# Performance work log

Measured on AMD Instinct MI355X. Metric: run time of the kernel, lower is better.

## Reference

```python
import math
import jax, jax.numpy as jnp
import numpy as np

L, C, FC, K, H, WIN, T, B = 6, 512, 2048, 3, 8, 4, 1024, 4
KC = C // H
EPS = 1e-4


def setup_inputs() -> dict:
    key = jax.random.key(0)
    ks = jax.random.split(key, 20)
    s = 0.05
    f = jnp.float32
    inp = {
        "x": jax.random.normal(ks[0], (B, C, T), f),
        "wq": jax.random.normal(ks[1], (L, C, C), f) * s,
        "bq": jnp.zeros((L, C), f),
        "wk": jax.random.normal(ks[2], (L, C, C), f) * s,
        "bk": jnp.zeros((L, C), f),
        "wv": jax.random.normal(ks[3], (L, C, C), f) * s,
        "bv": jnp.zeros((L, C), f),
        "wo": jax.random.normal(ks[4], (L, C, C), f) * s,
        "bo": jnp.zeros((L, C), f),
        "rel_k": jax.random.normal(ks[5], (L, 1, 2 * WIN + 1, KC), f) * (KC ** -0.5),
        "g1": jnp.ones((L, C), f),
        "be1": jnp.zeros((L, C), f),
        "w1": jax.random.normal(ks[6], (L, FC, C, K), f) * s,
        "bb1": jnp.zeros((L, FC), f),
        "w2": jax.random.normal(ks[7], (L, C, FC, K), f) * s,
        "bb2": jnp.zeros((L, C), f),
        "g2": jnp.ones((L, C), f),
        "be2": jnp.zeros((L, C), f),
    }
    return inp


def conv1d(x, w, b, pad):
    # x: [B,Cin,T], w: [Cout,Cin,K]
    y = jax.lax.conv_general_dilated(x, w, (1,), [(pad, pad)],
                                     dimension_numbers=("NCH", "OIH", "NCH"))
    return y + b[None, :, None]


def layer_norm(x, g, b):
    # normalize over channel dim (axis 1), matching the torch LayerNorm above
    m = jnp.mean(x, 1, keepdims=True)
    v = jnp.mean((x - m) ** 2, 1, keepdims=True)
    return (x - m) * jax.lax.rsqrt(v + EPS) * g[None, :, None] + b[None, :, None]


def get_relative_embeddings(rel, length):
    pad_len = max(length - (WIN + 1), 0)
    start = max(WIN + 1 - length, 0)
    if pad_len > 0:
        rel = jnp.pad(rel, ((0, 0), (pad_len, pad_len), (0, 0)), mode="edge")
    return rel[:, start:start + 2 * length - 1]


def rel_to_abs(x):
    # x: [b,h,l,2l-1] -> [b,h,l,l]  (Music-Transformer skew)
    b, h, l, _ = x.shape
    x = jnp.pad(x, ((0, 0), (0, 0), (0, 0), (0, 1)))          # [b,h,l,2l]
    x = x.reshape(b, h, l * 2 * l)
    x = jnp.pad(x, ((0, 0), (0, 0), (0, l - 1)))
    x = x.reshape(b, h, l + 1, 2 * l - 1)[:, :, :l, l - 1:]
    return x


def attention(x, wq, bq, wk, bk, wv, bv, wo, bo, rel_k):
    b, c, t = x.shape
    q = conv1d(x, wq[:, :, None], bq, 0).reshape(b, H, KC, t)
    k = conv1d(x, wk[:, :, None], bk, 0).reshape(b, H, KC, t)
    v = conv1d(x, wv[:, :, None], bv, 0).reshape(b, H, KC, t)
    scale = 1.0 / math.sqrt(KC)
    scores = jnp.einsum("bhdt,bhds->bhts", q, k) * scale      # [b,H,t,t]
    rel = get_relative_embeddings(rel_k, t)[0]                # [2t-1, KC] (heads_share)
    rel_logits = jnp.einsum("bhdt,md->bhtm", q * scale, rel)  # [b,H,t,2t-1]
    scores = scores + rel_to_abs(rel_logits)
    p = jax.nn.softmax(scores, axis=-1)
    out = jnp.einsum("bhts,bhds->bhdt", p, v).reshape(b, c, t)
    return conv1d(out, wo[:, :, None], bo, 0)


def reference(x, wq, bq, wk, bk, wv, bv, wo, bo, rel_k,
              g1, be1, w1, bb1, w2, bb2, g2, be2):
    for i in range(L):
        y = attention(x, wq[i], bq[i], wk[i], bk[i], wv[i], bv[i],
                      wo[i], bo[i], rel_k[i])
        x = layer_norm(x + y, g1[i], be1[i])
        y = conv1d(jax.nn.relu(conv1d(x, w1[i], bb1[i], K // 2)), w2[i], bb2[i], K // 2)
        x = layer_norm(x + y, g2[i], be2[i])
    return x
```

## Files before the change

kernel.cpp:

```cpp
#include <hip/hip_runtime.h>

constexpr int L  = 6;
constexpr int C  = 512;
constexpr int FC = 2048;
constexpr int H  = 8;
constexpr int KC = 64;
constexpr int T  = 1024;
constexpr int B  = 4;
#define SCALE 0.125f
#define LOG2E 1.4426950408889634f

typedef __bf16 bf16_t;
typedef __bf16 bf16x8 __attribute__((ext_vector_type(8)));
typedef float  f32x4  __attribute__((ext_vector_type(4)));

constexpr size_t OFF_XF    = 0;
constexpr size_t OFF_YF    = OFF_XF   + (size_t)B*T*C*4;
constexpr size_t OFF_XPAD  = OFF_YF   + (size_t)B*T*C*4;
constexpr size_t OFF_Q     = OFF_XPAD + (size_t)B*(T+2)*C*2;
constexpr size_t OFF_K     = OFF_Q    + (size_t)B*T*C*2;
constexpr size_t OFF_VT    = OFF_K    + (size_t)B*T*C*2;
constexpr size_t OFF_YA    = OFF_VT   + (size_t)B*T*C*2;
constexpr size_t OFF_MID   = OFF_YA   + (size_t)B*T*C*2;
constexpr size_t OFF_WQKVO = OFF_MID  + (size_t)B*(T+2)*FC*2;
constexpr size_t OFF_W1    = OFF_WQKVO+ (size_t)4*C*C*2;
constexpr size_t OFF_W2    = OFF_W1   + (size_t)3*FC*C*2;

__device__ __forceinline__ void gload_lds16(const bf16_t* g, bf16_t* l) {
    __builtin_amdgcn_global_load_lds((const __attribute__((address_space(1))) void*)g,
                                     (__attribute__((address_space(3))) void*)l, 16, 0, 0);
}

__global__ __launch_bounds__(256) void cvt4_kernel(const float* __restrict__ a,
                                                   const float* __restrict__ b,
                                                   const float* __restrict__ c,
                                                   const float* __restrict__ d,
                                                   bf16_t* __restrict__ out) {
    int i = blockIdx.x * 256 + threadIdx.x;
    int which = i >> 18;
    int idx   = i & ((1 << 18) - 1);
    const float* s = (which == 0) ? a : (which == 1) ? b : (which == 2) ? c : d;
    out[i] = (bf16_t)s[idx];
}

__global__ __launch_bounds__(256) void cvtw1_kernel(const float* __restrict__ w1, bf16_t* __restrict__ out) {
    int i = blockIdx.x * 256 + threadIdx.x;
    int j = i >> 20;
    int rem = i & ((1 << 20) - 1);
    int fc = rem >> 9, c = rem & 511;
    out[i] = (bf16_t)w1[fc * (C * 3) + c * 3 + j];
}

__global__ __launch_bounds__(256) void cvtw2_kernel(const float* __restrict__ w2, bf16_t* __restrict__ out) {
    int i = blockIdx.x * 256 + threadIdx.x;
    int j = i >> 20;
    int rem = i & ((1 << 20) - 1);
    int c = rem >> 11, fc = rem & 2047;
    out[i] = (bf16_t)w2[c * (FC * 3) + fc * 3 + j];
}

__global__ __launch_bounds__(256) void transpose_in(const float* __restrict__ x0,
                                                    float* __restrict__ xf,
                                                    bf16_t* __restrict__ xpad) {
    __shared__ float tile[32][33];
    int b = blockIdx.z, t0 = blockIdx.x * 32, c0 = blockIdx.y * 32;
    int tx = threadIdx.x, ty = threadIdx.y;
#pragma unroll
    for (int j = 0; j < 4; ++j)
        tile[ty + j * 8][tx] = x0[((size_t)b * C + c0 + ty + j * 8) * T + t0 + tx];
    __syncthreads();
#pragma unroll
    for (int j = 0; j < 4; ++j) {
        float v = tile[tx][ty + j * 8];
        long t = t0 + ty + j * 8;
        xf[((size_t)b * T + t) * C + c0 + tx] = v;
        xpad[((size_t)b * (T + 2) + t + 1) * C + c0 + tx] = (bf16_t)v;
    }
}

__global__ __launch_bounds__(256) void transpose_out(const float* __restrict__ xf,
                                                     float* __restrict__ out) {
    __shared__ float tile[32][33];
    int b = blockIdx.z, t0 = blockIdx.x * 32, c0 = blockIdx.y * 32;
    int tx = threadIdx.x, ty = threadIdx.y;
#pragma unroll
    for (int j = 0; j < 4; ++j)
        tile[ty + j * 8][tx] = xf[((size_t)b * T + t0 + ty + j * 8) * C + c0 + tx];
    __syncthreads();
#pragma unroll
    for (int j = 0; j < 4; ++j)
        out[((size_t)b * C + c0 + ty + j * 8) * T + t0 + tx] = tile[tx][ty + j * 8];
}

__global__ __launch_bounds__(256) void zero_pads(bf16_t* __restrict__ xpad, bf16_t* __restrict__ midp) {
    int i = blockIdx.x * 256 + threadIdx.x;
    if (i < 4096) {
        int b = i >> 10, r = (i >> 9) & 1, c = i & 511;
        xpad[((size_t)b * (T + 2) + (size_t)r * (T + 1)) * C + c] = (bf16_t)0.f;
    } else {
        int j = i - 4096;
        int b = j >> 12, r = (j >> 11) & 1, c = j & 2047;
        midp[((size_t)b * (T + 2) + (size_t)r * (T + 1)) * FC + c] = (bf16_t)0.f;
    }
}

template <int NP>
__global__ __launch_bounds__(256) void add_ln(float* __restrict__ x,
                                              const float* __restrict__ p0, const float* __restrict__ p1,
                                              const float* __restrict__ p2,
                                              const float* __restrict__ g, const float* __restrict__ be,
                                              bf16_t* __restrict__ xpad) {
    long bt = blockIdx.x;
    int tid = threadIdx.x;
    float* xr = x + bt * C;
    float v0 = xr[tid] + p0[bt * C + tid] + p1[bt * C + tid];
    float v1 = xr[tid + 256] + p0[bt * C + tid + 256] + p1[bt * C + tid + 256];
    if (NP == 3) { v0 += p2[bt * C + tid]; v1 += p2[bt * C + tid + 256]; }
    float s = v0 + v1, q = v0 * v0 + v1 * v1;
#pragma unroll
    for (int m = 1; m < 64; m <<= 1) { s += __shfl_xor(s, m); q += __shfl_xor(q, m); }
    __shared__ float ss[4], qq[4];
    int wid = tid >> 6;
    if ((tid & 63) == 0) { ss[wid] = s; qq[wid] = q; }
    __syncthreads();
    s = ss[0] + ss[1] + ss[2] + ss[3];
    q = qq[0] + qq[1] + qq[2] + qq[3];
    float mean = s * (1.f / C);
    float var = q * (1.f / C) - mean * mean;
    float rstd = rsqrtf(var + 1e-4f);
    float o0 = (v0 - mean) * rstd * g[tid] + be[tid];
    float o1 = (v1 - mean) * rstd * g[tid + 256] + be[tid + 256];
    xr[tid] = o0; xr[tid + 256] = o1;
    long b = bt >> 10, t = bt & (T - 1);
    bf16_t* xp = xpad + (b * (T + 2) + t + 1) * C;
    xp[tid] = (bf16_t)o0; xp[tid + 256] = (bf16_t)o1;
}

template <int OUTMODE, bool RELU, int NSPLIT, int IPT, int NTAPS>
__global__ __launch_bounds__(256) void gemm128(
    const bf16_t* __restrict__ A, long batchStrideA, int lda,
    const bf16_t* __restrict__ Bw, long tapStrideB, int ldb,
    const float* __restrict__ bias0, const float* __restrict__ bias1,
    const float* __restrict__ bias2,
    void* __restrict__ Dp, void* __restrict__ D1p, void* __restrict__ D2p,
    long batchStrideD, int ldd) {
    __shared__ bf16_t As[128 * 64];
    __shared__ bf16_t Bs[128 * 64];
    const int tid = threadIdx.x;
    const int lane = tid & 63, wid = tid >> 6;
    const int l15 = lane & 15, quad = lane >> 4;
    const int wy = wid >> 1, wx = wid & 1;
    const int nb = gridDim.z / NSPLIT;
    const int split = (NSPLIT > 1) ? ((int)blockIdx.z / nb) : 0;
    const int b = (int)blockIdx.z - split * nb;

    const bf16_t* Ab = A + (long)b * batchStrideA + (long)blockIdx.y * 128 * lda;
    const bf16_t* Bb = Bw + (long)blockIdx.x * 128 * ldb;

    const int lrow = lane >> 3;
    const int lcolsw = ((lane & 7) ^ lrow) * 8;

    f32x4 acc[4][4];
#pragma unroll
    for (int i = 0; i < 4; ++i)
#pragma unroll
        for (int j = 0; j < 4; ++j) acc[i][j] = (f32x4){0.f, 0.f, 0.f, 0.f};

    constexpr int itersAll = IPT * NTAPS;
    constexpr int per = itersAll / NSPLIT;
    const int it0 = split * per;

    for (int it = it0; it < it0 + per; ++it) {
        const int tap = (NTAPS == 1) ? 0 : (it / IPT);
        const int k0 = (it - tap * IPT) * 64;
        const bf16_t* At = Ab + (long)tap * lda + k0;
        const bf16_t* Bt = Bb + (long)tap * tapStrideB + k0;
        __syncthreads();
#pragma unroll
        for (int i = 0; i < 4; ++i) {
            int chunk = wid * 4 + i;
            int row = chunk * 8 + lrow;
            gload_lds16(At + (long)row * lda + lcolsw, As + chunk * 512 + lane * 8);
            gload_lds16(Bt + (long)row * ldb + lcolsw, Bs + chunk * 512 + lane * 8);
        }
        __syncthreads();
#pragma unroll
        for (int ks = 0; ks < 2; ++ks) {
            bf16x8 bfr[4], afr[4];
#pragma unroll
            for (int nt = 0; nt < 4; ++nt) {
                int row = wx * 64 + nt * 16 + l15;
                bfr[nt] = *(const bf16x8*)&Bs[row * 64 + (((ks * 4 + quad) ^ (l15 & 7)) * 8)];
            }
#pragma unroll
            for (int mt = 0; mt < 4; ++mt) {
                int row = wy * 64 + mt * 16 + l15;
                afr[mt] = *(const bf16x8*)&As[row * 64 + (((ks * 4 + quad) ^ (l15 & 7)) * 8)];
            }
#pragma unroll
            for (int mt = 0; mt < 4; ++mt)
#pragma unroll
                for (int nt = 0; nt < 4; ++nt)
                    acc[mt][nt] = __builtin_amdgcn_mfma_f32_16x16x32_bf16(afr[mt], bfr[nt], acc[mt][nt], 0, 0, 0);
        }
    }

    const long m0 = (long)blockIdx.y * 128 + wy * 64;
    const int n0g = (int)blockIdx.x * 128 + wx * 64;
#pragma unroll
    for (int mt = 0; mt < 4; ++mt) {
        long rowb = m0 + mt * 16 + quad * 4;
#pragma unroll
        for (int nt = 0; nt < 4; ++nt) {
            int col = n0g + nt * 16 + l15;
            if (OUTMODE == 0) {
                float bb = (split == 0) ? bias0[col] : 0.f;
                float* D = ((split == 0) ? (float*)Dp : (split == 1) ? (float*)D1p : (float*)D2p)
                           + (long)b * batchStrideD;
#pragma unroll
                for (int r = 0; r < 4; ++r) D[(rowb + r) * ldd + col] = acc[mt][nt][r] + bb;
            } else if (OUTMODE == 1) {
                float bb = bias0[col];
                bf16_t* D = (bf16_t*)Dp + (long)b * batchStrideD;
#pragma unroll
                for (int r = 0; r < 4; ++r) {
                    float v = acc[mt][nt][r] + bb;
                    if (RELU) v = fmaxf(v, 0.f);
                    D[(rowb + r) * ldd + col] = (bf16_t)v;
                }
            } else {
                int which = col >> 9, cl = col & 511;
                const float* bp = (which == 0) ? bias0 : (which == 1) ? bias1 : bias2;
                float bb = bp[cl];
                if (which < 2) {
                    bf16_t* D = (bf16_t*)((which == 0) ? Dp : D1p) + (long)b * T * C;
#pragma unroll
                    for (int r = 0; r < 4; ++r) D[(rowb + r) * C + cl] = (bf16_t)(acc[mt][nt][r] + bb);
                } else {
                    bf16_t* D = (bf16_t*)D2p + (long)b * C * T;
                    union { bf16_t h[4]; uint2 u; } pk;
#pragma unroll
                    for (int r = 0; r < 4; ++r) pk.h[r] = (bf16_t)(acc[mt][nt][r] + bb);
                    *(uint2*)(D + (long)cl * T + rowb) = pk.u;
                }
            }
        }
    }
}

__global__ __launch_bounds__(256) void attn_kernel(const bf16_t* __restrict__ q,
                                                   const bf16_t* __restrict__ k,
                                                   const bf16_t* __restrict__ vT,
                                                   const float* __restrict__ relk,
                                                   bf16_t* __restrict__ y) {
    const int b = blockIdx.z, h = blockIdx.y;
    const int qt0 = blockIdx.x * 64;
    __shared__ bf16_t qps[64 * 72];
    __shared__ bf16_t ktb[2][64 * 64];
    __shared__ bf16_t vtb[2][64 * 64];
    __shared__ float  rl[64][12];

    const int tid = threadIdx.x;
    const int lane = tid & 63, wid = tid >> 6;
    const int l15 = lane & 15, quad = lane >> 4;
    const int lrow = lane >> 3;
    const int su   = ((lane & 7) ^ lrow) * 8;

    const bf16_t* qbase = q + ((size_t)(b * T + qt0)) * C + h * 64;
    const bf16_t* kbs = k + ((size_t)(b * T)) * C + h * 64;
    const bf16_t* vbs = vT + ((size_t)(b * C + h * 64)) * T;
#pragma unroll
    for (int i = 0; i < 2; ++i) {
        int chunk = wid * 2 + i;
        int row = chunk * 8 + lrow;
        gload_lds16(qbase + (long)row * C + su, qps + chunk * 512 + lane * 8);
        gload_lds16(kbs + (long)row * C + su, ktb[0] + chunk * 512 + lane * 8);
        gload_lds16(vbs + (long)row * T + su, vtb[0] + chunk * 512 + lane * 8);
    }
    __syncthreads();

    for (int i = tid; i < 64 * 9; i += 256) {
        int r = i / 9, j = i - r * 9;
        float acc = 0.f;
#pragma unroll
        for (int d = 0; d < 64; ++d)
            acc += (float)qps[r * 64 + ((d >> 3) ^ (r & 7)) * 8 + (d & 7)] * relk[j * 64 + d];
        rl[r][j] = acc * (SCALE * LOG2E);
    }

    bf16x8 af[2];
#pragma unroll
    for (int ks = 0; ks < 2; ++ks) {
        int r = wid * 16 + l15;
        af[ks] = *(const bf16x8*)&qps[r * 64 + (((ks * 4 + quad) ^ (r & 7)) * 8)];
    }

    float m_i[4], l_i[4];
    f32x4 o[4];
#pragma unroll
    for (int r = 0; r < 4; ++r) { m_i[r] = -1e30f; l_i[r] = 0.f; }
#pragma unroll
    for (int dn = 0; dn < 4; ++dn) o[dn] = (f32x4){0.f, 0.f, 0.f, 0.f};

    for (int st = 0; st < T / 64; ++st) {
        __syncthreads();
        if (st < T / 64 - 1) {
            const bf16_t* kb = kbs + (size_t)(st + 1) * 64 * C;
            const bf16_t* vb = vbs + (st + 1) * 64;
            bf16_t* kd = ktb[(st + 1) & 1];
            bf16_t* vd = vtb[(st + 1) & 1];
#pragma unroll
            for (int i = 0; i < 2; ++i) {
                int chunk = wid * 2 + i;
                int row = chunk * 8 + lrow;
                gload_lds16(kb + (long)row * C + su, kd + chunk * 512 + lane * 8);
                gload_lds16(vb + (long)row * T + su, vd + chunk * 512 + lane * 8);
            }
        }
        const bf16_t* ktc = ktb[st & 1];
        const bf16_t* vtc = vtb[st & 1];

        f32x4 sc[4];
#pragma unroll
        for (int nt = 0; nt < 4; ++nt) {
            f32x4 a = (f32x4){0.f, 0.f, 0.f, 0.f};
#pragma unroll
            for (int ks = 0; ks < 2; ++ks) {
                int rr = nt * 16 + l15;
                bf16x8 bfr = *(const bf16x8*)&ktc[rr * 64 + (((ks * 4 + quad) ^ (l15 & 7)) * 8)];
                a = __builtin_amdgcn_mfma_f32_16x16x32_bf16(af[ks], bfr, a, 0, 0, 0);
            }
            sc[nt] = a;
        }

#pragma unroll
        for (int nt = 0; nt < 4; ++nt)
#pragma unroll
            for (int r = 0; r < 4; ++r) {
                int row = wid * 16 + quad * 4 + r;
                int j = (st * 64 + nt * 16 + l15) - (qt0 + row) + 4;
                j = j < 0 ? 0 : (j > 8 ? 8 : j);
                sc[nt][r] = sc[nt][r] * (SCALE * LOG2E) + rl[row][j];
            }

        float alpha[4];
#pragma unroll
        for (int r = 0; r < 4; ++r) {
            float mx = fmaxf(fmaxf(sc[0][r], sc[1][r]), fmaxf(sc[2][r], sc[3][r]));
#pragma unroll
            for (int d = 1; d < 16; d <<= 1) mx = fmaxf(mx, __shfl_xor(mx, d));
            float mn = fmaxf(m_i[r], mx);
            alpha[r] = exp2f(m_i[r] - mn);
            m_i[r] = mn;
        }
#pragma unroll
        for (int r = 0; r < 4; ++r) {
            float rs = 0.f;
#pragma unroll
            for (int nt = 0; nt < 4; ++nt) {
                float p = exp2f(sc[nt][r] - m_i[r]);
                sc[nt][r] = p;
                rs += p;
            }
#pragma unroll
            for (int d = 1; d < 16; d <<= 1) rs += __shfl_xor(rs, d);
            l_i[r] = l_i[r] * alpha[r] + rs;
        }
#pragma unroll
        for (int dn = 0; dn < 4; ++dn)
#pragma unroll
            for (int r = 0; r < 4; ++r) o[dn][r] *= alpha[r];

#pragma unroll
        for (int nt = 0; nt < 4; ++nt)
#pragma unroll
            for (int r = 0; r < 4; ++r)
                qps[(wid * 16 + quad * 4 + r) * 72 + nt * 16 + l15] = (bf16_t)sc[nt][r];

        bf16x8 pa[2];
#pragma unroll
        for (int ks = 0; ks < 2; ++ks)
            pa[ks] = *(const bf16x8*)&qps[(wid * 16 + l15) * 72 + ks * 32 + quad * 8];
#pragma unroll
        for (int dn = 0; dn < 4; ++dn)
#pragma unroll
            for (int ks = 0; ks < 2; ++ks) {
                int rr = dn * 16 + l15;
                bf16x8 vf = *(const bf16x8*)&vtc[rr * 64 + (((ks * 4 + quad) ^ (l15 & 7)) * 8)];
                o[dn] = __builtin_amdgcn_mfma_f32_16x16x32_bf16(pa[ks], vf, o[dn], 0, 0, 0);
            }
    }

    bf16_t* yb = y + ((size_t)(b * T + qt0)) * C + h * 64;
#pragma unroll
    for (int r = 0; r < 4; ++r) {
        float linv = 1.f / l_i[r];
        int row = wid * 16 + quad * 4 + r;
#pragma unroll
        for (int dn = 0; dn < 4; ++dn)
            yb[(long)row * C + dn * 16 + l15] = (bf16_t)(o[dn][r] * linv);
    }
}

extern "C" void kernel_launch(void* const* d_in, const int* in_sizes, int n_in,
                              void* d_out, int out_size, void* d_ws, size_t ws_size,
                              hipStream_t stream) {
    const float* x0  = (const float*)d_in[0];
    const float* wq  = (const float*)d_in[1];
    const float* bq  = (const float*)d_in[2];
    const float* wk  = (const float*)d_in[3];
    const float* bk  = (const float*)d_in[4];
    const float* wv  = (const float*)d_in[5];
    const float* bv  = (const float*)d_in[6];
    const float* wo  = (const float*)d_in[7];
    const float* bo  = (const float*)d_in[8];
    const float* rlk = (const float*)d_in[9];
    const float* g1  = (const float*)d_in[10];
    const float* be1 = (const float*)d_in[11];
    const float* w1  = (const float*)d_in[12];
    const float* bb1 = (const float*)d_in[13];
    const float* w2  = (const float*)d_in[14];
    const float* bb2 = (const float*)d_in[15];
    const float* g2  = (const float*)d_in[16];
    const float* be2 = (const float*)d_in[17];

    char* ws = (char*)d_ws;
    float*  xf    = (float*)(ws + OFF_XF);
    float*  yf    = (float*)(ws + OFF_YF);
    float*  yf2   = (float*)(ws + OFF_Q);
    float*  yf3   = (float*)(ws + OFF_VT);
    bf16_t* xpad  = (bf16_t*)(ws + OFF_XPAD);
    bf16_t* qb    = (bf16_t*)(ws + OFF_Q);
    bf16_t* kb    = (bf16_t*)(ws + OFF_K);
    bf16_t* vTb   = (bf16_t*)(ws + OFF_VT);
    bf16_t* yab   = (bf16_t*)(ws + OFF_YA);
    bf16_t* midp  = (bf16_t*)(ws + OFF_MID);
    bf16_t* wqkvo = (bf16_t*)(ws + OFF_WQKVO);
    bf16_t* w1b   = (bf16_t*)(ws + OFF_W1);
    bf16_t* w2b   = (bf16_t*)(ws + OFF_W2);

    transpose_in<<<dim3(T / 32, C / 32, B), dim3(32, 8), 0, stream>>>(x0, xf, xpad);
    zero_pads<<<80, 256, 0, stream>>>(xpad, midp);

    for (int l = 0; l < L; ++l) {
        cvt4_kernel<<<4 * C * C / 256, 256, 0, stream>>>(wq + (size_t)l * C * C, wk + (size_t)l * C * C,
                                                         wv + (size_t)l * C * C, wo + (size_t)l * C * C, wqkvo);
        cvtw1_kernel<<<3 * FC * C / 256, 256, 0, stream>>>(w1 + (size_t)l * FC * C * 3, w1b);
        cvtw2_kernel<<<3 * C * FC / 256, 256, 0, stream>>>(w2 + (size_t)l * C * FC * 3, w2b);

        gemm128<3, false, 1, 8, 1><<<dim3(1536 / 128, T / 128, B), 256, 0, stream>>>(
            xpad + C, (long)(T + 2) * C, C, wqkvo, 0, C,
            bq + l * C, bk + l * C, bv + l * C,
            (void*)qb, (void*)kb, (void*)vTb, 0, 0);

        attn_kernel<<<dim3(T / 64, H, B), 256, 0, stream>>>(qb, kb, vTb, rlk + (size_t)l * 9 * KC, yab);

        gemm128<0, false, 2, 8, 1><<<dim3(C / 128, T / 128, 2 * B), 256, 0, stream>>>(
            yab, (long)T * C, C, wqkvo + 3 * C * C, 0, C,
            bo + l * C, nullptr, nullptr,
            (void*)yf, (void*)yf2, nullptr, (long)T * C, C);

        add_ln<2><<<B * T, 256, 0, stream>>>(xf, yf, yf2, nullptr, g1 + l * C, be1 + l * C, xpad);

        gemm128<1, true, 1, 8, 3><<<dim3(FC / 128, T / 128, B), 256, 0, stream>>>(
            xpad, (long)(T + 2) * C, C, w1b, (long)FC * C, C,
            bb1 + l * FC, nullptr, nullptr,
            (void*)(midp + FC), nullptr, nullptr, (long)(T + 2) * FC, FC);

        gemm128<0, false, 3, 32, 3><<<dim3(C / 128, T / 128, 3 * B), 256, 0, stream>>>(
            midp, (long)(T + 2) * FC, FC, w2b, (long)C * FC, FC,
            bb2 + l * C, nullptr, nullptr,
            (void*)yf, (void*)yf2, (void*)yf3, (long)T * C, C);

        add_ln<3><<<B * T, 256, 0, stream>>>(xf, yf, yf2, yf3, g2 + l * C, be2 + l * C, xpad);
    }

    transpose_out<<<dim3(T / 32, C / 32, B), dim3(32, 8), 0, stream>>>(xf, (float*)d_out);
}
```

Before: 1.308 ms.

## Split attention over two key halves and combine partial softmax results

The attention kernel now splits the key/value sequence into two halves across the grid z dimension, so twice as many blocks run. Each block writes unnormalized fp32 partial outputs plus running max and sum, and a new combine kernel merges them into the bf16 output. V is no longer double-buffered, and an extra barrier separates its load from the PV step. The partial buffers reuse the FFN mid-activation workspace, so the mid pad rows are re-zeroed inside the first add_ln. The cost is an extra kernel launch and extra fp32 traffic for the partial results.

```diff
diff --git a/kernel.cpp b/kernel.cpp
--- a/kernel.cpp
+++ b/kernel.cpp
@@ -104,14 +104,21 @@
     }
 }
 
-template <int NP>
+template <int NP, bool ZPAD>
 __global__ __launch_bounds__(256) void add_ln(float* __restrict__ x,
                                               const float* __restrict__ p0, const float* __restrict__ p1,
                                               const float* __restrict__ p2,
                                               const float* __restrict__ g, const float* __restrict__ be,
-                                              bf16_t* __restrict__ xpad) {
+                                              bf16_t* __restrict__ xpad, bf16_t* __restrict__ midp) {
     long bt = blockIdx.x;
     int tid = threadIdx.x;
+    if (ZPAD) {
+        if (bt < 64) {
+            int idx = (int)bt * 256 + tid;
+            int bb = idx >> 12, r = (idx >> 11) & 1, cc = idx & 2047;
+            midp[((size_t)bb * (T + 2) + (size_t)r * (T + 1)) * FC + cc] = (bf16_t)0.f;
+        }
+    }
     float* xr = x + bt * C;
     float v0 = xr[tid] + p0[bt * C + tid] + p1[bt * C + tid];
     float v1 = xr[tid + 256] + p0[bt * C + tid + 256] + p1[bt * C + tid + 256];
@@ -252,12 +259,16 @@
                                                    const bf16_t* __restrict__ k,
                                                    const bf16_t* __restrict__ vT,
                                                    const float* __restrict__ relk,
-                                                   bf16_t* __restrict__ y) {
-    const int b = blockIdx.z, h = blockIdx.y;
+                                                   float* __restrict__ op,
+                                                   float* __restrict__ mb,
+                                                   float* __restrict__ lb) {
+    const int z = blockIdx.z;
+    const int b = z % B, half = z / B;
+    const int h = blockIdx.y;
     const int qt0 = blockIdx.x * 64;
     __shared__ bf16_t qps[64 * 72];
     __shared__ bf16_t ktb[2][64 * 64];
-    __shared__ bf16_t vtb[2][64 * 64];
+    __shared__ bf16_t vtb[64 * 64];
     __shared__ float  rl[64][12];
 
     const int tid = threadIdx.x;
@@ -267,15 +278,15 @@
     const int su   = ((lane & 7) ^ lrow) * 8;
 
     const bf16_t* qbase = q + ((size_t)(b * T + qt0)) * C + h * 64;
-    const bf16_t* kbs = k + ((size_t)(b * T)) * C + h * 64;
-    const bf16_t* vbs = vT + ((size_t)(b * C + h * 64)) * T;
+    const bf16_t* kbs = k + ((size_t)(b * T + half * 512)) * C + h * 64;
+    const bf16_t* vbs = vT + ((size_t)(b * C + h * 64)) * T + half * 512;
+
 #pragma unroll
     for (int i = 0; i < 2; ++i) {
         int chunk = wid * 2 + i;
         int row = chunk * 8 + lrow;
         gload_lds16(qbase + (long)row * C + su, qps + chunk * 512 + lane * 8);
         gload_lds16(kbs + (long)row * C + su, ktb[0] + chunk * 512 + lane * 8);
-        gload_lds16(vbs + (long)row * T + su, vtb[0] + chunk * 512 + lane * 8);
     }
     __syncthreads();
 
@@ -302,23 +313,25 @@
 #pragma unroll
     for (int dn = 0; dn < 4; ++dn) o[dn] = (f32x4){0.f, 0.f, 0.f, 0.f};
 
-    for (int st = 0; st < T / 64; ++st) {
+    for (int st = 0; st < 8; ++st) {
         __syncthreads();
-        if (st < T / 64 - 1) {
-            const bf16_t* kb = kbs + (size_t)(st + 1) * 64 * C;
-            const bf16_t* vb = vbs + (st + 1) * 64;
-            bf16_t* kd = ktb[(st + 1) & 1];
-            bf16_t* vd = vtb[(st + 1) & 1];
+        {
+            const bf16_t* vb = vbs + st * 64;
 #pragma unroll
             for (int i = 0; i < 2; ++i) {
-                int chunk = wid * 2 + i;
-                int row = chunk * 8 + lrow;
-                gload_lds16(kb + (long)row * C + su, kd + chunk * 512 + lane * 8);
-                gload_lds16(vb + (long)row * T + su, vd + chunk * 512 + lane * 8);
+                int chunk = wid * 2 + i, row = chunk * 8 + lrow;
+                gload_lds16(vb + (long)row * T + su, vtb + chunk * 512 + lane * 8);
+            }
+        }
+        if (st < 7) {
+            const bf16_t* kb2 = kbs + (size_t)(st + 1) * 64 * C;
+#pragma unroll
+            for (int i = 0; i < 2; ++i) {
+                int chunk = wid * 2 + i, row = chunk * 8 + lrow;
+                gload_lds16(kb2 + (long)row * C + su, ktb[(st + 1) & 1] + chunk * 512 + lane * 8);
             }
         }
         const bf16_t* ktc = ktb[st & 1];
-        const bf16_t* vtc = vtb[st & 1];
 
         f32x4 sc[4];
 #pragma unroll
@@ -338,7 +351,7 @@
 #pragma unroll
             for (int r = 0; r < 4; ++r) {
                 int row = wid * 16 + quad * 4 + r;
-                int j = (st * 64 + nt * 16 + l15) - (qt0 + row) + 4;
+                int j = (half * 512 + st * 64 + nt * 16 + l15) - (qt0 + row) + 4;
                 j = j < 0 ? 0 : (j > 8 ? 8 : j);
                 sc[nt][r] = sc[nt][r] * (SCALE * LOG2E) + rl[row][j];
             }
@@ -371,6 +384,8 @@
 #pragma unroll
             for (int r = 0; r < 4; ++r) o[dn][r] *= alpha[r];
 
+        __syncthreads();
+
 #pragma unroll
         for (int nt = 0; nt < 4; ++nt)
 #pragma unroll
@@ -386,20 +401,45 @@
 #pragma unroll
             for (int ks = 0; ks < 2; ++ks) {
                 int rr = dn * 16 + l15;
-                bf16x8 vf = *(const bf16x8*)&vtc[rr * 64 + (((ks * 4 + quad) ^ (l15 & 7)) * 8)];
+                bf16x8 vf = *(const bf16x8*)&vtb[rr * 64 + (((ks * 4 + quad) ^ (l15 & 7)) * 8)];
                 o[dn] = __builtin_amdgcn_mfma_f32_16x16x32_bf16(pa[ks], vf, o[dn], 0, 0, 0);
             }
     }
 
-    bf16_t* yb = y + ((size_t)(b * T + qt0)) * C + h * 64;
+    float* opb = op + ((size_t)((half * B + b) * T + qt0)) * C + h * 64;
+    float* mptr = mb + ((size_t)((half * B + b) * H + h)) * T + qt0;
+    float* lptr = lb + ((size_t)((half * B + b) * H + h)) * T + qt0;
 #pragma unroll
     for (int r = 0; r < 4; ++r) {
-        float linv = 1.f / l_i[r];
         int row = wid * 16 + quad * 4 + r;
 #pragma unroll
         for (int dn = 0; dn < 4; ++dn)
-            yb[(long)row * C + dn * 16 + l15] = (bf16_t)(o[dn][r] * linv);
-    }
+            opb[(long)row * C + dn * 16 + l15] = o[dn][r];
+        if (l15 == 0) { mptr[row] = m_i[r]; lptr[row] = l_i[r]; }
+    }
+}
+
+__global__ __launch_bounds__(256) void attn_combine(const float* __restrict__ op,
+                                                    const float* __restrict__ mb,
+                                                    const float* __restrict__ lb,
+                                                    bf16_t* __restrict__ y) {
+    int bt = blockIdx.x;
+    int b = bt >> 10, t = bt & (T - 1);
+    int tid = threadIdx.x;
+    int h = tid >> 5;
+    size_t mi0 = ((size_t)(b)*H + h) * T + t;
+    size_t mi1 = ((size_t)(B + b) * H + h) * T + t;
+    float m0 = mb[mi0], l0 = lb[mi0];
+    float m1 = mb[mi1], l1 = lb[mi1];
+    float mm = fmaxf(m0, m1);
+    float a0 = exp2f(m0 - mm), a1 = exp2f(m1 - mm);
+    float linv = 1.f / (l0 * a0 + l1 * a1);
+    float2 o0 = *((const float2*)(op + ((size_t)b * T + t) * C) + tid);
+    float2 o1 = *((const float2*)(op + ((size_t)(B + b) * T + t) * C) + tid);
+    union { bf16_t h2[2]; unsigned u; } pk;
+    pk.h2[0] = (bf16_t)((o0.x * a0 + o1.x * a1) * linv);
+    pk.h2[1] = (bf16_t)((o0.y * a0 + o1.y * a1) * linv);
+    ((unsigned*)(y + ((size_t)(b * T + t)) * C))[tid] = pk.u;
 }
 
 extern "C" void kernel_launch(void* const* d_in, const int* in_sizes, int n_in,
@@ -438,6 +478,9 @@
     bf16_t* wqkvo = (bf16_t*)(ws + OFF_WQKVO);
     bf16_t* w1b   = (bf16_t*)(ws + OFF_W1);
     bf16_t* w2b   = (bf16_t*)(ws + OFF_W2);
+    float*  opart = (float*)(ws + OFF_MID);
+    float*  mpart = (float*)(ws + OFF_YF);
+    float*  lpart = mpart + (size_t)2 * B * H * T;
 
     transpose_in<<<dim3(T / 32, C / 32, B), dim3(32, 8), 0, stream>>>(x0, xf, xpad);
     zero_pads<<<80, 256, 0, stream>>>(xpad, midp);
@@ -453,14 +496,16 @@
             bq + l * C, bk + l * C, bv + l * C,
             (void*)qb, (void*)kb, (void*)vTb, 0, 0);
 
-        attn_kernel<<<dim3(T / 64, H, B), 256, 0, stream>>>(qb, kb, vTb, rlk + (size_t)l * 9 * KC, yab);
+        attn_kernel<<<dim3(T / 64, H, 2 * B), 256, 0, stream>>>(qb, kb, vTb, rlk + (size_t)l * 9 * KC,
+                                                                opart, mpart, lpart);
+        attn_combine<<<B * T, 256, 0, stream>>>(opart, mpart, lpart, yab);
 
         gemm128<0, false, 2, 8, 1><<<dim3(C / 128, T / 128, 2 * B), 256, 0, stream>>>(
             yab, (long)T * C, C, wqkvo + 3 * C * C, 0, C,
             bo + l * C, nullptr, nullptr,
             (void*)yf, (void*)yf2, nullptr, (long)T * C, C);
 
-        add_ln<2><<<B * T, 256, 0, stream>>>(xf, yf, yf2, nullptr, g1 + l * C, be1 + l * C, xpad);
+        add_ln<2, true><<<B * T, 256, 0, stream>>>(xf, yf, yf2, nullptr, g1 + l * C, be1 + l * C, xpad, midp);
 
         gemm128<1, true, 1, 8, 3><<<dim3(FC / 128, T / 128, B), 256, 0, stream>>>(
             xpad, (long)(T + 2) * C, C, w1b, (long)FC * C, C,
@@ -472,7 +517,7 @@
             bb2 + l * C, nullptr, nullptr,
             (void*)yf, (void*)yf2, (void*)yf3, (long)T * C, C);
 
-        add_ln<3><<<B * T, 256, 0, stream>>>(xf, yf, yf2, yf3, g2 + l * C, be2 + l * C, xpad);
+        add_ln<3, false><<<B * T, 256, 0, stream>>>(xf, yf, yf2, yf3, g2 + l * C, be2 + l * C, xpad, nullptr);
     }
 
     transpose_out<<<dim3(T / 32, C / 32, B), dim3(32, 8), 0, stream>>>(xf, (float*)d_out);
```

Result: slower. 1.344 ms (+2.8%).

## Transpose attention MFMA operands so each lane owns one query row

Applied to the files above, without the earlier changes.

The attention kernel swaps the A/B operands of both MFMAs, so each lane holds one query row and the softmax max/sum reductions need only two cross-lane shuffles instead of four per row. It also skips the per-element relative-position lookup for tiles entirely outside the window, using the clamped edge bias directly. P and the output are written with packed 64-bit stores instead of scalar stores, and a barrier is added after the relative-logit setup. The risks are a new branch in the inner loop and correctness depending on the transposed fragment layouts lining up.

```diff
diff --git a/kernel.cpp b/kernel.cpp
--- a/kernel.cpp
+++ b/kernel.cpp
@@ -269,6 +269,7 @@
     const bf16_t* qbase = q + ((size_t)(b * T + qt0)) * C + h * 64;
     const bf16_t* kbs = k + ((size_t)(b * T)) * C + h * 64;
     const bf16_t* vbs = vT + ((size_t)(b * C + h * 64)) * T;
+
 #pragma unroll
     for (int i = 0; i < 2; ++i) {
         int chunk = wid * 2 + i;
@@ -287,34 +288,34 @@
             acc += (float)qps[r * 64 + ((d >> 3) ^ (r & 7)) * 8 + (d & 7)] * relk[j * 64 + d];
         rl[r][j] = acc * (SCALE * LOG2E);
     }
-
+    __syncthreads();
+
+    const int qrow = wid * 16 + l15;
     bf16x8 af[2];
 #pragma unroll
-    for (int ks = 0; ks < 2; ++ks) {
-        int r = wid * 16 + l15;
-        af[ks] = *(const bf16x8*)&qps[r * 64 + (((ks * 4 + quad) ^ (r & 7)) * 8)];
-    }
-
-    float m_i[4], l_i[4];
+    for (int ks = 0; ks < 2; ++ks)
+        af[ks] = *(const bf16x8*)&qps[qrow * 64 + (((ks * 4 + quad) ^ (qrow & 7)) * 8)];
+    const float rl0 = rl[qrow][0], rl8 = rl[qrow][8];
+
+    float m_i = -1e30f, l_i = 0.f;
     f32x4 o[4];
 #pragma unroll
-    for (int r = 0; r < 4; ++r) { m_i[r] = -1e30f; l_i[r] = 0.f; }
-#pragma unroll
     for (int dn = 0; dn < 4; ++dn) o[dn] = (f32x4){0.f, 0.f, 0.f, 0.f};
+
+    bf16_t* myP = qps + wid * (16 * 72);
 
     for (int st = 0; st < T / 64; ++st) {
         __syncthreads();
         if (st < T / 64 - 1) {
-            const bf16_t* kb = kbs + (size_t)(st + 1) * 64 * C;
-            const bf16_t* vb = vbs + (st + 1) * 64;
+            const bf16_t* kb2 = kbs + (size_t)(st + 1) * 64 * C;
+            const bf16_t* vb2 = vbs + (st + 1) * 64;
             bf16_t* kd = ktb[(st + 1) & 1];
             bf16_t* vd = vtb[(st + 1) & 1];
 #pragma unroll
             for (int i = 0; i < 2; ++i) {
-                int chunk = wid * 2 + i;
-                int row = chunk * 8 + lrow;
-                gload_lds16(kb + (long)row * C + su, kd + chunk * 512 + lane * 8);
-                gload_lds16(vb + (long)row * T + su, vd + chunk * 512 + lane * 8);
+                int chunk = wid * 2 + i, row = chunk * 8 + lrow;
+                gload_lds16(kb2 + (long)row * C + su, kd + chunk * 512 + lane * 8);
+                gload_lds16(vb2 + (long)row * T + su, vd + chunk * 512 + lane * 8);
             }
         }
         const bf16_t* ktc = ktb[st & 1];
@@ -327,78 +328,88 @@
 #pragma unroll
             for (int ks = 0; ks < 2; ++ks) {
                 int rr = nt * 16 + l15;
-                bf16x8 bfr = *(const bf16x8*)&ktc[rr * 64 + (((ks * 4 + quad) ^ (l15 & 7)) * 8)];
-                a = __builtin_amdgcn_mfma_f32_16x16x32_bf16(af[ks], bfr, a, 0, 0, 0);
+                bf16x8 kfr = *(const bf16x8*)&ktc[rr * 64 + (((ks * 4 + quad) ^ (l15 & 7)) * 8)];
+                a = __builtin_amdgcn_mfma_f32_16x16x32_bf16(kfr, af[ks], a, 0, 0, 0);
             }
             sc[nt] = a;
         }
 
+        const int base = st * 64 - qt0 - wid * 16;
+        if (base >= 32) {
+#pragma unroll
+            for (int nt = 0; nt < 4; ++nt)
+#pragma unroll
+                for (int r = 0; r < 4; ++r) sc[nt][r] = sc[nt][r] * (SCALE * LOG2E) + rl8;
+        } else if (base <= -80) {
+#pragma unroll
+            for (int nt = 0; nt < 4; ++nt)
+#pragma unroll
+                for (int r = 0; r < 4; ++r) sc[nt][r] = sc[nt][r] * (SCALE * LOG2E) + rl0;
+        } else {
+#pragma unroll
+            for (int nt = 0; nt < 4; ++nt)
+#pragma unroll
+                for (int r = 0; r < 4; ++r) {
+                    int j = base + nt * 16 + quad * 4 + r - l15 + 4;
+                    j = j < 0 ? 0 : (j > 8 ? 8 : j);
+                    sc[nt][r] = sc[nt][r] * (SCALE * LOG2E) + rl[qrow][j];
+                }
+        }
+
+        float mx = fmaxf(fmaxf(fmaxf(sc[0][0], sc[0][1]), fmaxf(sc[0][2], sc[0][3])),
+                         fmaxf(fmaxf(sc[1][0], sc[1][1]), fmaxf(sc[1][2], sc[1][3])));
+        mx = fmaxf(mx, fmaxf(fmaxf(fmaxf(sc[2][0], sc[2][1]), fmaxf(sc[2][2], sc[2][3])),
+                             fmaxf(fmaxf(sc[3][0], sc[3][1]), fmaxf(sc[3][2], sc[3][3]))));
+        mx = fmaxf(mx, __shfl_xor(mx, 16));
+        mx = fmaxf(mx, __shfl_xor(mx, 32));
+        float mn = fmaxf(m_i, mx);
+        float alpha = exp2f(m_i - mn);
+        m_i = mn;
+        float rs = 0.f;
 #pragma unroll
         for (int nt = 0; nt < 4; ++nt)
 #pragma unroll
             for (int r = 0; r < 4; ++r) {
-                int row = wid * 16 + quad * 4 + r;
-                int j = (st * 64 + nt * 16 + l15) - (qt0 + row) + 4;
-                j = j < 0 ? 0 : (j > 8 ? 8 : j);
-                sc[nt][r] = sc[nt][r] * (SCALE * LOG2E) + rl[row][j];
-            }
-
-        float alpha[4];
-#pragma unroll
-        for (int r = 0; r < 4; ++r) {
-            float mx = fmaxf(fmaxf(sc[0][r], sc[1][r]), fmaxf(sc[2][r], sc[3][r]));
-#pragma unroll
-            for (int d = 1; d < 16; d <<= 1) mx = fmaxf(mx, __shfl_xor(mx, d));
-            float mn = fmaxf(m_i[r], mx);
-            alpha[r] = exp2f(m_i[r] - mn);
-            m_i[r] = mn;
-        }
-#pragma unroll
-        for (int r = 0; r < 4; ++r) {
-            float rs = 0.f;
-#pragma unroll
-            for (int nt = 0; nt < 4; ++nt) {
-                float p = exp2f(sc[nt][r] - m_i[r]);
+                float p = exp2f(sc[nt][r] - m_i);
                 sc[nt][r] = p;
                 rs += p;
             }
-#pragma unroll
-            for (int d = 1; d < 16; d <<= 1) rs += __shfl_xor(rs, d);
-            l_i[r] = l_i[r] * alpha[r] + rs;
-        }
-#pragma unroll
-        for (int dn = 0; dn < 4; ++dn)
-#pragma unroll
-            for (int r = 0; r < 4; ++r) o[dn][r] *= alpha[r];
-
-#pragma unroll
-        for (int nt = 0; nt < 4; ++nt)
-#pragma unroll
-            for (int r = 0; r < 4; ++r)
-                qps[(wid * 16 + quad * 4 + r) * 72 + nt * 16 + l15] = (bf16_t)sc[nt][r];
-
-        bf16x8 pa[2];
+        rs += __shfl_xor(rs, 16);
+        rs += __shfl_xor(rs, 32);
+        l_i = l_i * alpha + rs;
+#pragma unroll
+        for (int dn = 0; dn < 4; ++dn) o[dn] *= alpha;
+
+#pragma unroll
+        for (int nt = 0; nt < 4; ++nt) {
+            union { bf16_t hh[4]; uint2 u; } pk;
+#pragma unroll
+            for (int r = 0; r < 4; ++r) pk.hh[r] = (bf16_t)sc[nt][r];
+            *(uint2*)&myP[l15 * 72 + nt * 16 + quad * 4] = pk.u;
+        }
+
+        bf16x8 pb[2];
 #pragma unroll
         for (int ks = 0; ks < 2; ++ks)
-            pa[ks] = *(const bf16x8*)&qps[(wid * 16 + l15) * 72 + ks * 32 + quad * 8];
+            pb[ks] = *(const bf16x8*)&myP[l15 * 72 + ks * 32 + quad * 8];
 #pragma unroll
         for (int dn = 0; dn < 4; ++dn)
 #pragma unroll
             for (int ks = 0; ks < 2; ++ks) {
                 int rr = dn * 16 + l15;
                 bf16x8 vf = *(const bf16x8*)&vtc[rr * 64 + (((ks * 4 + quad) ^ (l15 & 7)) * 8)];
-                o[dn] = __builtin_amdgcn_mfma_f32_16x16x32_bf16(pa[ks], vf, o[dn], 0, 0, 0);
-            }
-    }
-
-    bf16_t* yb = y + ((size_t)(b * T + qt0)) * C + h * 64;
-#pragma unroll
-    for (int r = 0; r < 4; ++r) {
-        float linv = 1.f / l_i[r];
-        int row = wid * 16 + quad * 4 + r;
-#pragma unroll
-        for (int dn = 0; dn < 4; ++dn)
-            yb[(long)row * C + dn * 16 + l15] = (bf16_t)(o[dn][r] * linv);
+                o[dn] = __builtin_amdgcn_mfma_f32_16x16x32_bf16(vf, pb[ks], o[dn], 0, 0, 0);
+            }
+    }
+
+    float linv = 1.f / l_i;
+    bf16_t* yb = y + ((size_t)(b * T + qt0 + qrow)) * C + h * 64;
+#pragma unroll
+    for (int dn = 0; dn < 4; ++dn) {
+        union { bf16_t hh[4]; uint2 u; } pk;
+#pragma unroll
+        for (int r = 0; r < 4; ++r) pk.hh[r] = (bf16_t)(o[dn][r] * linv);
+        *(uint2*)(yb + dn * 16 + quad * 4) = pk.u;
     }
 }
 
```

Result: faster. 1.239 ms (-5.3%).
